# Performance work log

Hardware: AMD Instinct MI355X
Metric: run time of the kernel (lower is better)

The kernel has to match this reference:

```python
import jax, jax.numpy as jnp
import numpy as np

B, L, D, H, DH, M = 2, 2048, 512, 8, 2048, 128  # batch, seq, d_model, heads, d_hidden, max_rel_pos
HD = D // H
EPS = 1e-5


def _ln(x, w, b):
    mu = jnp.mean(x, axis=-1, keepdims=True)
    var = jnp.mean((x - mu) ** 2, axis=-1, keepdims=True)
    return (x - mu) * jax.lax.rsqrt(var + EPS) * w + b


def setup_inputs() -> dict:
    key = jax.random.key(0)
    ks = jax.random.split(key, 8)
    s = 0.02  # init std for weights
    return {
        "x": jax.random.normal(ks[0], (B, L, D), jnp.float32),
        "ln1_w": jnp.ones((D,), jnp.float32),
        "ln1_b": jnp.zeros((D,), jnp.float32),
        "qkv_w": jax.random.normal(ks[1], (D, 3 * D), jnp.float32) * s,
        "qkv_b": jnp.zeros((3 * D,), jnp.float32),
        "out_w": jax.random.normal(ks[2], (D, D), jnp.float32) * s,
        "out_b": jnp.zeros((D,), jnp.float32),
        "rel_bias": jax.random.normal(ks[3], (H, 2 * M - 1), jnp.float32) * s,
        "gamma1": 1e-4 * jnp.ones((D,), jnp.float32),
        "ln2_w": jnp.ones((D,), jnp.float32),
        "ln2_b": jnp.zeros((D,), jnp.float32),
        "ffn_in_w": jax.random.normal(ks[4], (D, 2 * DH), jnp.float32) * s,
        "ffn_in_b": jnp.zeros((2 * DH,), jnp.float32),
        "ffn_out_w": jax.random.normal(ks[5], (DH, D), jnp.float32) * s,
        "ffn_out_b": jnp.zeros((D,), jnp.float32),
        "gamma2": 1e-4 * jnp.ones((D,), jnp.float32),
    }


def _forward(x, ln1_w, ln1_b, qkv_w, qkv_b, out_w, out_b, rel_bias, gamma1,
             ln2_w, ln2_b, ffn_in_w, ffn_in_b, ffn_out_w, ffn_out_b, gamma2):
    b, l, d = x.shape
    # --- PreNorm attention with T5-style relative position bias ---
    h = _ln(x, ln1_w, ln1_b)
    qkv = h @ qkv_w + qkv_b                           # [B, L, 3D]
    q, k, v = jnp.split(qkv, 3, axis=-1)
    q = q.reshape(b, l, H, HD)
    k = k.reshape(b, l, H, HD)
    v = v.reshape(b, l, H, HD)
    scale = 1.0 / jnp.sqrt(jnp.asarray(HD, x.dtype))
    scores = jnp.einsum("bqhd,bkhd->bhqk", q, k) * scale   # [B, H, L, L]
    # relative position bias: clip(i - j) indexed into learned table
    ctx = jnp.arange(l)[:, None] - jnp.arange(l)[None, :]
    ctx = jnp.clip(ctx, -(M - 1), M - 1) + (M - 1)          # [L, L] in [0, 2M-2]
    rel = rel_bias[:, ctx]                                  # [H, L, L]
    scores = scores + rel[None]
    attn = jax.nn.softmax(scores, axis=-1)
    o = jnp.einsum("bhqk,bkhd->bqhd", attn, v).reshape(b, l, d)
    o = o @ out_w + out_b
    x = x + o * gamma1                                      # LayerScale residual
    # --- PreNorm GEGLU FFN ---
    h2 = _ln(x, ln2_w, ln2_b)
    ab = h2 @ ffn_in_w + ffn_in_b                           # [B, L, 2*DH]
    a, bgate = jnp.split(ab, 2, axis=-1)
    f = jax.nn.gelu(bgate, approximate=False) * a
    f = f @ ffn_out_w + ffn_out_b
    x = x + f * gamma2
    return x, attn


def reference(x, ln1_w, ln1_b, qkv_w, qkv_b, out_w, out_b, rel_bias, gamma1,
              ln2_w, ln2_b, ffn_in_w, ffn_in_b, ffn_out_w, ffn_out_b, gamma2):
    return _forward(x, ln1_w, ln1_b, qkv_w, qkv_b, out_w, out_b, rel_bias, gamma1,
                    ln2_w, ln2_b, ffn_in_w, ffn_in_b, ffn_out_w, ffn_out_b, gamma2)
```

## Files before the change

### kernel.cpp

```cpp
#include <hip/hip_runtime.h>
#include <math.h>

typedef __attribute__((ext_vector_type(4))) float f32x4;
typedef __attribute__((ext_vector_type(8))) short bf16x8;
typedef __attribute__((ext_vector_type(4))) short s16x4;

#if __has_builtin(__builtin_amdgcn_exp2f)
#define EXP2(x) __builtin_amdgcn_exp2f(x)
#else
#define EXP2(x) exp2f(x)
#endif

__device__ __forceinline__ unsigned short f2bf(float f) {
  union { float f; unsigned u; } v; v.f = f;
  return (unsigned short)((v.u + 0x7fffu + ((v.u >> 16) & 1u)) >> 16);
}

__global__ void ln_kernel(const float* __restrict__ in, const float* __restrict__ w,
                          const float* __restrict__ b, unsigned short* __restrict__ out) {
  __shared__ float sh[4];
  const int t = threadIdx.x;
  const float* p = in + (size_t)blockIdx.x * 512;
  float a0 = p[t], a1 = p[t + 256];
  float s = a0 + a1;
#pragma unroll
  for (int o = 32; o; o >>= 1) s += __shfl_down(s, o);
  if ((t & 63) == 0) sh[t >> 6] = s;
  __syncthreads();
  s = sh[0] + sh[1] + sh[2] + sh[3];
  float mu = s * (1.0f / 512.0f);
  float d0 = a0 - mu, d1 = a1 - mu;
  float q = d0 * d0 + d1 * d1;
  __syncthreads();
#pragma unroll
  for (int o = 32; o; o >>= 1) q += __shfl_down(q, o);
  if ((t & 63) == 0) sh[t >> 6] = q;
  __syncthreads();
  q = sh[0] + sh[1] + sh[2] + sh[3];
  float rstd = rsqrtf(q * (1.0f / 512.0f) + 1e-5f);
  unsigned short* po = out + (size_t)blockIdx.x * 512;
  po[t]       = f2bf(d0 * rstd * w[t] + b[t]);
  po[t + 256] = f2bf(d1 * rstd * w[t + 256] + b[t + 256]);
}

__global__ void transpose_all(const float* __restrict__ w0, unsigned short* __restrict__ o0,
                              const float* __restrict__ w1, unsigned short* __restrict__ o1,
                              const float* __restrict__ w2, unsigned short* __restrict__ o2,
                              const float* __restrict__ w3, unsigned short* __restrict__ o3) {
  __shared__ float tile[32][33];
  int idx = blockIdx.x;
  const float* in; unsigned short* out; int ldi, ldo, nx;
  if (idx < 768)        { in = w0; out = o0; ldi = 1536; ldo = 512;  nx = 48; }
  else if (idx < 1024)  { idx -= 768;  in = w1; out = o1; ldi = 512;  ldo = 512;  nx = 16; }
  else if (idx < 3072)  { idx -= 1024; in = w2; out = o2; ldi = 4096; ldo = 512;  nx = 128; }
  else                  { idx -= 3072; in = w3; out = o3; ldi = 512;  ldo = 2048; nx = 16; }
  const int tx = threadIdx.x & 31;
  const int ty = threadIdx.x >> 5;
  const int n0 = (idx % nx) * 32, k0 = (idx / nx) * 32;
#pragma unroll
  for (int i = 0; i < 4; ++i)
    tile[ty + i * 8][tx] = in[(size_t)(k0 + ty + i * 8) * ldi + n0 + tx];
  __syncthreads();
#pragma unroll
  for (int i = 0; i < 4; ++i)
    out[(size_t)(n0 + ty + i * 8) * ldo + k0 + tx] = f2bf(tile[tx][ty + i * 8]);
}

template <int WM, int WN, int TM, int TN, int EPI>
__global__ __launch_bounds__(256) void gemm_bb(
    const unsigned short* __restrict__ A, const unsigned short* __restrict__ Bt,
    float* __restrict__ C, unsigned short* __restrict__ Cbf, unsigned short* __restrict__ Vt,
    int K, int lda, int ldb, int ldc,
    const float* __restrict__ bias, const float* __restrict__ resid,
    const float* __restrict__ gamma) {
  constexpr int BM = WM * TM * 16;
  constexpr int BN = WN * TN * 16;
  constexpr int LDS_STRIDE = 72;
  __shared__ short As[BM * LDS_STRIDE];
  __shared__ short Bs[BN * LDS_STRIDE];

  const int tid = threadIdx.x;
  const int m0 = blockIdx.y * BM, n0 = blockIdx.x * BN;
  const int w = tid >> 6, lane = tid & 63;
  const int wm = w / WN, wn = w % WN;
  const int lrow = lane & 15, lq = lane >> 4;

  f32x4 acc[TM][TN];
#pragma unroll
  for (int i = 0; i < TM; ++i)
#pragma unroll
    for (int j = 0; j < TN; ++j) acc[i][j] = (f32x4){0.f, 0.f, 0.f, 0.f};

  for (int k0 = 0; k0 < K; k0 += 64) {
    __syncthreads();
#pragma unroll
    for (int it = 0; it < BM / 32; ++it) {
      int c = it * 256 + tid;
      int row = c >> 3, col = (c & 7) << 3;
      *(bf16x8*)(As + row * LDS_STRIDE + col) =
          *(const bf16x8*)(A + (size_t)(m0 + row) * lda + k0 + col);
    }
#pragma unroll
    for (int it = 0; it < BN / 32; ++it) {
      int c = it * 256 + tid;
      int row = c >> 3, col = (c & 7) << 3;
      *(bf16x8*)(Bs + row * LDS_STRIDE + col) =
          *(const bf16x8*)(Bt + (size_t)(n0 + row) * ldb + k0 + col);
    }
    __syncthreads();

    bf16x8 af[TM][2], bf[TN][2];
#pragma unroll
    for (int mi = 0; mi < TM; ++mi)
#pragma unroll
      for (int c = 0; c < 2; ++c)
        af[mi][c] = *(const bf16x8*)(As + (wm * TM * 16 + mi * 16 + lrow) * LDS_STRIDE + c * 32 + lq * 8);
#pragma unroll
    for (int nj = 0; nj < TN; ++nj)
#pragma unroll
      for (int c = 0; c < 2; ++c)
        bf[nj][c] = *(const bf16x8*)(Bs + (wn * TN * 16 + nj * 16 + lrow) * LDS_STRIDE + c * 32 + lq * 8);
#pragma unroll
    for (int mi = 0; mi < TM; ++mi)
#pragma unroll
      for (int nj = 0; nj < TN; ++nj)
#pragma unroll
        for (int c = 0; c < 2; ++c)
          acc[mi][nj] = __builtin_amdgcn_mfma_f32_16x16x32_bf16(af[mi][c], bf[nj][c], acc[mi][nj], 0, 0, 0);
  }

#pragma unroll
  for (int mi = 0; mi < TM; ++mi) {
#pragma unroll
    for (int nj = 0; nj < TN; ++nj) {
      int gm0 = m0 + wm * TM * 16 + mi * 16 + lq * 4;
      int gn = n0 + wn * TN * 16 + nj * 16 + lrow;
      if constexpr (EPI == 4) {
        if (gn >= 1024) {
          int h = (gn - 1024) >> 6, dd = (gn - 1024) & 63;
          int bb = gm0 >> 11, l0 = gm0 & 2047;
          float bs = bias[gn];
          s16x4 r4 = {(short)f2bf(acc[mi][nj][0] + bs), (short)f2bf(acc[mi][nj][1] + bs),
                      (short)f2bf(acc[mi][nj][2] + bs), (short)f2bf(acc[mi][nj][3] + bs)};
          *(s16x4*)(Vt + ((size_t)(bb * 8 + h) * 64 + dd) * 2048 + l0) = r4;
          continue;
        }
      }
#pragma unroll
      for (int r = 0; r < 4; ++r) {
        int gm = gm0 + r;
        size_t idx = (size_t)gm * ldc + gn;
        float v = acc[mi][nj][r];
        if constexpr (EPI == 0) {
          C[idx] = v + bias[gn];
        } else if constexpr (EPI == 4) {
          float u = v + bias[gn];
          Cbf[idx] = f2bf(gn < 512 ? u * 0.18033688011112042f : u);
        } else {
          C[idx] = resid[idx] + (v + bias[gn]) * gamma[gn];
        }
      }
    }
  }
}

__global__ __launch_bounds__(256) void ffn1_gate_kernel(
    const unsigned short* __restrict__ A, const unsigned short* __restrict__ Bt,
    unsigned short* __restrict__ F, const float* __restrict__ bias) {
  constexpr int LDS_STRIDE = 72;
  __shared__ short As[128 * LDS_STRIDE];
  __shared__ short Bs[64 * LDS_STRIDE];
  __shared__ short Bs2[64 * LDS_STRIDE];

  const int tid = threadIdx.x;
  const int n0 = blockIdx.x * 64, m0 = blockIdx.y * 128;
  const int w = tid >> 6, lane = tid & 63;
  const int wm = w >> 1, wn = w & 1;
  const int lrow = lane & 15, lq = lane >> 4;

  f32x4 acca[4][2], accb[4][2];
#pragma unroll
  for (int i = 0; i < 4; ++i)
#pragma unroll
    for (int j = 0; j < 2; ++j) {
      acca[i][j] = (f32x4){0.f, 0.f, 0.f, 0.f};
      accb[i][j] = (f32x4){0.f, 0.f, 0.f, 0.f};
    }

  for (int k0 = 0; k0 < 512; k0 += 64) {
    __syncthreads();
#pragma unroll
    for (int it = 0; it < 4; ++it) {
      int c = it * 256 + tid;
      int row = c >> 3, col = (c & 7) << 3;
      *(bf16x8*)(As + row * LDS_STRIDE + col) =
          *(const bf16x8*)(A + (size_t)(m0 + row) * 512 + k0 + col);
    }
#pragma unroll
    for (int it = 0; it < 2; ++it) {
      int c = it * 256 + tid;
      int row = c >> 3, col = (c & 7) << 3;
      *(bf16x8*)(Bs + row * LDS_STRIDE + col) =
          *(const bf16x8*)(Bt + (size_t)(n0 + row) * 512 + k0 + col);
      *(bf16x8*)(Bs2 + row * LDS_STRIDE + col) =
          *(const bf16x8*)(Bt + (size_t)(2048 + n0 + row) * 512 + k0 + col);
    }
    __syncthreads();

    bf16x8 af[4][2], ba[2][2], bb[2][2];
#pragma unroll
    for (int mi = 0; mi < 4; ++mi)
#pragma unroll
      for (int c = 0; c < 2; ++c)
        af[mi][c] = *(const bf16x8*)(As + (wm * 64 + mi * 16 + lrow) * LDS_STRIDE + c * 32 + lq * 8);
#pragma unroll
    for (int nj = 0; nj < 2; ++nj)
#pragma unroll
      for (int c = 0; c < 2; ++c) {
        ba[nj][c] = *(const bf16x8*)(Bs + (wn * 32 + nj * 16 + lrow) * LDS_STRIDE + c * 32 + lq * 8);
        bb[nj][c] = *(const bf16x8*)(Bs2 + (wn * 32 + nj * 16 + lrow) * LDS_STRIDE + c * 32 + lq * 8);
      }
#pragma unroll
    for (int mi = 0; mi < 4; ++mi)
#pragma unroll
      for (int nj = 0; nj < 2; ++nj)
#pragma unroll
        for (int c = 0; c < 2; ++c) {
          acca[mi][nj] = __builtin_amdgcn_mfma_f32_16x16x32_bf16(af[mi][c], ba[nj][c], acca[mi][nj], 0, 0, 0);
          accb[mi][nj] = __builtin_amdgcn_mfma_f32_16x16x32_bf16(af[mi][c], bb[nj][c], accb[mi][nj], 0, 0, 0);
        }
  }

#pragma unroll
  for (int mi = 0; mi < 4; ++mi)
#pragma unroll
    for (int nj = 0; nj < 2; ++nj) {
      int gm0 = m0 + wm * 64 + mi * 16 + lq * 4;
      int gn = n0 + wn * 32 + nj * 16 + lrow;
#pragma unroll
      for (int r = 0; r < 4; ++r) {
        float a = acca[mi][nj][r] + bias[gn];
        float bg = accb[mi][nj][r] + bias[2048 + gn];
        float g = 0.5f * bg * (1.0f + erff(bg * 0.70710678118654752f));
        F[(size_t)(gm0 + r) * 2048 + gn] = f2bf(g * a);
      }
    }
}

__global__ __launch_bounds__(256, 8) void attn_fused(
    const unsigned short* __restrict__ qkvbf, const unsigned short* __restrict__ vt,
    const float* __restrict__ rel, float* __restrict__ attn, unsigned short* __restrict__ o) {
  __shared__ __align__(16) float scr[3072];
  __shared__ float erel[256];
  __shared__ float rsum[16];
  __shared__ float rinv[16];

  const int tid = threadIdx.x;
  const int flat = blockIdx.y * 128 + blockIdx.x;
  const int swz = (flat & 7) * 256 + (flat >> 3);
  const int bh = swz >> 7;
  const int m0 = (swz & 127) * 16;
  const int b = bh >> 3, h = bh & 7;

  const int w = tid >> 6, lane = tid & 63;
  const int lrow = lane & 15, lq = lane >> 4;

  const unsigned short* qb = qkvbf + (size_t)(b * 2048) * 1536 + h * 64;
  const unsigned short* kb = qb + 512;
  const unsigned short* vb = vt + (size_t)bh * 64 * 2048;
  float* ab = attn + (size_t)bh * 2048 * 2048;
  const float* relh = rel + h * 255;

  if (tid < 16) rsum[tid] = 0.f;
  if (tid < 255) erel[tid] = __expf(relh[tid]);

  bf16x8 qf[2];
#pragma unroll
  for (int c = 0; c < 2; ++c)
    qf[c] = *(const bf16x8*)(qb + (size_t)(m0 + lrow) * 1536 + c * 32 + lq * 8);

  const unsigned short* krow = kb + (size_t)(w * 32 + lrow) * 1536 + lq * 8;
  const unsigned short* vrow = vb + (size_t)lrow * 2048 + w * 32 + lq * 8;

  __syncthreads();

  float psum[4] = {0.f, 0.f, 0.f, 0.f};
  const int dbase = (m0 + lq * 4) - (w * 32 + lrow);
  for (int t = 0; t < 16; ++t) {
    const int kt0 = t * 128;
    f32x4 acc[2];
#pragma unroll
    for (int nj = 0; nj < 2; ++nj) acc[nj] = (f32x4){0.f, 0.f, 0.f, 0.f};
#pragma unroll
    for (int c = 0; c < 2; ++c) {
      bf16x8 kf[2];
#pragma unroll
      for (int nj = 0; nj < 2; ++nj)
        kf[nj] = *(const bf16x8*)(krow + (size_t)(kt0 + nj * 16) * 1536 + c * 32);
#pragma unroll
      for (int nj = 0; nj < 2; ++nj)
        acc[nj] = __builtin_amdgcn_mfma_f32_16x16x32_bf16(qf[c], kf[nj], acc[nj], 0, 0, 0);
    }
    const int Dt = m0 - kt0;
    if (Dt >= 254 || Dt <= -144) {
      float ec = erel[Dt >= 254 ? 254 : 0];
#pragma unroll
      for (int r = 0; r < 4; ++r)
        psum[r] += ec * (EXP2(acc[0][r]) + EXP2(acc[1][r]));
    } else {
#pragma unroll
      for (int nj = 0; nj < 2; ++nj) {
        int d0 = dbase - kt0 - nj * 16;
#pragma unroll
        for (int r = 0; r < 4; ++r) {
          int d = d0 + r;
          d = d < -127 ? -127 : (d > 127 ? 127 : d);
          psum[r] += EXP2(acc[nj][r]) * erel[d + 127];
        }
      }
    }
  }
#pragma unroll
  for (int off = 1; off < 16; off <<= 1)
#pragma unroll
    for (int r = 0; r < 4; ++r) psum[r] += __shfl_xor(psum[r], off);
  if (lrow == 0) {
#pragma unroll
    for (int r = 0; r < 4; ++r) atomicAdd(&rsum[lq * 4 + r], psum[r]);
  }
  __syncthreads();
  if (tid < 16) rinv[tid] = 1.0f / rsum[tid];
  __syncthreads();
  float rv[4];
#pragma unroll
  for (int r = 0; r < 4; ++r) rv[r] = rinv[lq * 4 + r];

  f32x4 oacc[4];
#pragma unroll
  for (int nj = 0; nj < 4; ++nj) oacc[nj] = (f32x4){0.f, 0.f, 0.f, 0.f};
  float* pw = scr + w * 512;
  const int wsw = lq << 3;
  const int rsw = ((lrow >> 2) & 3) << 3;

  for (int t = 0; t < 16; ++t) {
    const int kt0 = t * 128;
    f32x4 acc[2];
#pragma unroll
    for (int nj = 0; nj < 2; ++nj) acc[nj] = (f32x4){0.f, 0.f, 0.f, 0.f};
#pragma unroll
    for (int c = 0; c < 2; ++c) {
      bf16x8 kf[2];
#pragma unroll
      for (int nj = 0; nj < 2; ++nj)
        kf[nj] = *(const bf16x8*)(krow + (size_t)(kt0 + nj * 16) * 1536 + c * 32);
#pragma unroll
      for (int nj = 0; nj < 2; ++nj)
        acc[nj] = __builtin_amdgcn_mfma_f32_16x16x32_bf16(qf[c], kf[nj], acc[nj], 0, 0, 0);
    }

    const int Dt = m0 - kt0;
    if (Dt >= 254 || Dt <= -144) {
      float ec = erel[Dt >= 254 ? 254 : 0];
#pragma unroll
      for (int r = 0; r < 4; ++r) {
        float fr = ec * rv[r];
        int prow = lq * 4 + r;
#pragma unroll
        for (int nj = 0; nj < 2; ++nj)
          pw[prow * 32 + ((nj * 16 + lrow) ^ wsw)] = EXP2(acc[nj][r]) * fr;
      }
    } else {
#pragma unroll
      for (int r = 0; r < 4; ++r) {
        int prow = lq * 4 + r;
        int d0 = dbase - kt0 + r;
#pragma unroll
        for (int nj = 0; nj < 2; ++nj) {
          int d = d0 - nj * 16;
          d = d < -127 ? -127 : (d > 127 ? 127 : d);
          pw[prow * 32 + ((nj * 16 + lrow) ^ wsw)] = EXP2(acc[nj][r]) * (erel[d + 127] * rv[r]);
        }
      }
    }

#pragma unroll
    for (int it = 0; it < 2; ++it) {
      int unit = it * 64 + lane;
      int row = unit >> 3, cg = unit & 7;
      f32x4 vv = *(const f32x4*)(pw + row * 32 + ((cg * 4) ^ (((row >> 2) & 3) << 3)));
      __builtin_nontemporal_store(
          vv, (f32x4*)(ab + (size_t)(m0 + row) * 2048 + kt0 + w * 32 + cg * 4));
    }

    {
      const float* pp = pw + lrow * 32 + ((lq * 8) ^ rsw);
      f32x4 pa = *(const f32x4*)pp;
      f32x4 pb = *(const f32x4*)(pp + 4);
      bf16x8 ap = {(short)f2bf(pa[0]), (short)f2bf(pa[1]), (short)f2bf(pa[2]), (short)f2bf(pa[3]),
                   (short)f2bf(pb[0]), (short)f2bf(pb[1]), (short)f2bf(pb[2]), (short)f2bf(pb[3])};
      bf16x8 bv[4];
#pragma unroll
      for (int nj = 0; nj < 4; ++nj)
        bv[nj] = *(const bf16x8*)(vrow + (size_t)(nj * 16) * 2048 + kt0);
#pragma unroll
      for (int nj = 0; nj < 4; ++nj)
        oacc[nj] = __builtin_amdgcn_mfma_f32_16x16x32_bf16(ap, bv[nj], oacc[nj], 0, 0, 0);
    }
  }

  __syncthreads();
  if (w > 0) {
#pragma unroll
    for (int nj = 0; nj < 4; ++nj)
#pragma unroll
      for (int r = 0; r < 4; ++r)
        scr[(w - 1) * 1024 + (lq * 4 + r) * 64 + nj * 16 + lrow] = oacc[nj][r];
  }
  __syncthreads();
  if (w == 0) {
#pragma unroll
    for (int nj = 0; nj < 4; ++nj)
#pragma unroll
      for (int r = 0; r < 4; ++r) {
        int ii = (lq * 4 + r) * 64 + nj * 16 + lrow;
        float v = oacc[nj][r] + scr[ii] + scr[1024 + ii] + scr[2048 + ii];
        o[(size_t)(b * 2048 + m0 + lq * 4 + r) * 512 + h * 64 + nj * 16 + lrow] = f2bf(v);
      }
  }
}

extern "C" void kernel_launch(void* const* d_in, const int* in_sizes, int n_in,
                              void* d_out, int out_size, void* d_ws, size_t ws_size,
                              hipStream_t stream) {
  (void)in_sizes; (void)n_in; (void)out_size; (void)ws_size;
  const float* x        = (const float*)d_in[0];
  const float* ln1_w    = (const float*)d_in[1];
  const float* ln1_b    = (const float*)d_in[2];
  const float* qkv_w    = (const float*)d_in[3];
  const float* qkv_b    = (const float*)d_in[4];
  const float* out_w    = (const float*)d_in[5];
  const float* out_b    = (const float*)d_in[6];
  const float* rel_bias = (const float*)d_in[7];
  const float* gamma1   = (const float*)d_in[8];
  const float* ln2_w    = (const float*)d_in[9];
  const float* ln2_b    = (const float*)d_in[10];
  const float* ffn_in_w = (const float*)d_in[11];
  const float* ffn_in_b = (const float*)d_in[12];
  const float* ffn_out_w  = (const float*)d_in[13];
  const float* ffn_out_b  = (const float*)d_in[14];
  const float* gamma2   = (const float*)d_in[15];

  float* x_out = (float*)d_out;
  float* attn  = x_out + (size_t)2 * 2048 * 512;

  float* ws  = (float*)d_ws;
  float* x1  = ws;
  unsigned short* h_bf  = (unsigned short*)(x1 + 2097152);
  unsigned short* o_bf  = h_bf + 2097152;
  unsigned short* f_bf  = o_bf + 2097152;
  unsigned short* qkvbf = f_bf;
  unsigned short* bt_qkv  = f_bf + 8388608;
  unsigned short* bt_out  = bt_qkv + 786432;
  unsigned short* bt_ffn1 = bt_out + 262144;
  unsigned short* bt_ffn2 = bt_ffn1 + 2097152;
  unsigned short* vt      = bt_ffn2 + 1048576;

  transpose_all<<<4096, 256, 0, stream>>>(qkv_w, bt_qkv, out_w, bt_out,
                                          ffn_in_w, bt_ffn1, ffn_out_w, bt_ffn2);

  ln_kernel<<<4096, 256, 0, stream>>>(x, ln1_w, ln1_b, h_bf);

  gemm_bb<2, 2, 4, 2, 4><<<dim3(24, 32, 1), 256, 0, stream>>>(
      h_bf, bt_qkv, nullptr, qkvbf, vt, 512, 512, 512, 1536, qkv_b, nullptr, nullptr);

  attn_fused<<<dim3(128, 16, 1), 256, 0, stream>>>(qkvbf, vt, rel_bias, attn, o_bf);

  gemm_bb<2, 2, 2, 2, 3><<<dim3(8, 64, 1), 256, 0, stream>>>(
      o_bf, bt_out, x1, nullptr, nullptr, 512, 512, 512, 512, out_b, x, gamma1);

  ln_kernel<<<4096, 256, 0, stream>>>(x1, ln2_w, ln2_b, h_bf);

  ffn1_gate_kernel<<<dim3(32, 32, 1), 256, 0, stream>>>(h_bf, bt_ffn1, f_bf, ffn_in_b);

  gemm_bb<2, 2, 2, 2, 3><<<dim3(8, 64, 1), 256, 0, stream>>>(
      f_bf, bt_ffn2, x_out, nullptr, nullptr, 2048, 2048, 2048, 512, ffn_out_b, x1, gamma2);
}
```

Before: 583.7 us.

## Enlarge attention tile to 32 query rows with 2x2 warp layout and K prefetch

The fused attention kernel now processes 32 query rows per block instead of 16. Its four waves are arranged 2x2: two row groups, each splitting the 128-key tile into two 64-key halves. K fragments are double-buffered in registers so the next tile's loads are issued before the current tile's MFMAs, and the final reduction across waves merges only two partials. This halves redundant K/V reads per query row and hides load latency. In exchange it uses more registers, which is why launch bounds drop to 4 blocks per CU, and the grid halves.

After: 591.9 us. About the same (+1.4%).

```diff
diff --git a/kernel.cpp b/kernel.cpp
--- a/kernel.cpp
+++ b/kernel.cpp
@@ -247,22 +247,23 @@
     }
 }
 
-__global__ __launch_bounds__(256, 8) void attn_fused(
+__global__ __launch_bounds__(256, 4) void attn_fused(
     const unsigned short* __restrict__ qkvbf, const unsigned short* __restrict__ vt,
     const float* __restrict__ rel, float* __restrict__ attn, unsigned short* __restrict__ o) {
-  __shared__ __align__(16) float scr[3072];
+  __shared__ __align__(16) float p_f32[4 * 16 * 64];
   __shared__ float erel[256];
-  __shared__ float rsum[16];
-  __shared__ float rinv[16];
+  __shared__ float rsum[32];
+  __shared__ float rinv[32];
 
   const int tid = threadIdx.x;
-  const int flat = blockIdx.y * 128 + blockIdx.x;
-  const int swz = (flat & 7) * 256 + (flat >> 3);
-  const int bh = swz >> 7;
-  const int m0 = (swz & 127) * 16;
+  const int flat = blockIdx.y * 64 + blockIdx.x;
+  const int swz = (flat & 7) * 128 + (flat >> 3);
+  const int bh = swz >> 6;
+  const int m0 = (swz & 63) * 32;
   const int b = bh >> 3, h = bh & 7;
 
   const int w = tid >> 6, lane = tid & 63;
+  const int wm = w >> 1, wn = w & 1;
   const int lrow = lane & 15, lq = lane >> 4;
 
   const unsigned short* qb = qkvbf + (size_t)(b * 2048) * 1536 + h * 64;
@@ -271,45 +272,53 @@
   float* ab = attn + (size_t)bh * 2048 * 2048;
   const float* relh = rel + h * 255;
 
-  if (tid < 16) rsum[tid] = 0.f;
+  if (tid < 32) rsum[tid] = 0.f;
   if (tid < 255) erel[tid] = __expf(relh[tid]);
 
   bf16x8 qf[2];
 #pragma unroll
   for (int c = 0; c < 2; ++c)
-    qf[c] = *(const bf16x8*)(qb + (size_t)(m0 + lrow) * 1536 + c * 32 + lq * 8);
-
-  const unsigned short* krow = kb + (size_t)(w * 32 + lrow) * 1536 + lq * 8;
-  const unsigned short* vrow = vb + (size_t)lrow * 2048 + w * 32 + lq * 8;
-
-  __syncthreads();
+    qf[c] = *(const bf16x8*)(qb + (size_t)(m0 + wm * 16 + lrow) * 1536 + c * 32 + lq * 8);
+
+  const unsigned short* krow = kb + (size_t)(wn * 64 + lrow) * 1536 + lq * 8;
+  const unsigned short* vrow = vb + (size_t)lrow * 2048 + wn * 64 + lq * 8;
+
+  __syncthreads();
+
+  auto LDK = [&](int t, bf16x8 (&kf)[2][4]) {
+#pragma unroll
+    for (int c = 0; c < 2; ++c)
+#pragma unroll
+      for (int nj = 0; nj < 4; ++nj)
+        kf[c][nj] = *(const bf16x8*)(krow + (size_t)(t * 128 + nj * 16) * 1536 + c * 32);
+  };
 
   float psum[4] = {0.f, 0.f, 0.f, 0.f};
-  const int dbase = (m0 + lq * 4) - (w * 32 + lrow);
-  for (int t = 0; t < 16; ++t) {
+  const int dbase = (m0 + wm * 16 + lq * 4) - (wn * 64 + lrow);
+
+  auto P1 = [&](int t, bf16x8 (&kf)[2][4]) {
     const int kt0 = t * 128;
-    f32x4 acc[2];
-#pragma unroll
-    for (int nj = 0; nj < 2; ++nj) acc[nj] = (f32x4){0.f, 0.f, 0.f, 0.f};
-#pragma unroll
-    for (int c = 0; c < 2; ++c) {
-      bf16x8 kf[2];
-#pragma unroll
-      for (int nj = 0; nj < 2; ++nj)
-        kf[nj] = *(const bf16x8*)(krow + (size_t)(kt0 + nj * 16) * 1536 + c * 32);
-#pragma unroll
-      for (int nj = 0; nj < 2; ++nj)
-        acc[nj] = __builtin_amdgcn_mfma_f32_16x16x32_bf16(qf[c], kf[nj], acc[nj], 0, 0, 0);
-    }
+    f32x4 acc[4];
+#pragma unroll
+    for (int nj = 0; nj < 4; ++nj) acc[nj] = (f32x4){0.f, 0.f, 0.f, 0.f};
+#pragma unroll
+    for (int c = 0; c < 2; ++c)
+#pragma unroll
+      for (int nj = 0; nj < 4; ++nj)
+        acc[nj] = __builtin_amdgcn_mfma_f32_16x16x32_bf16(qf[c], kf[c][nj], acc[nj], 0, 0, 0);
     const int Dt = m0 - kt0;
-    if (Dt >= 254 || Dt <= -144) {
-      float ec = erel[Dt >= 254 ? 254 : 0];
-#pragma unroll
-      for (int r = 0; r < 4; ++r)
-        psum[r] += ec * (EXP2(acc[0][r]) + EXP2(acc[1][r]));
+    if (Dt >= 256 || Dt <= -160) {
+      float ec = erel[Dt >= 256 ? 254 : 0];
+#pragma unroll
+      for (int r = 0; r < 4; ++r) {
+        float s = 0.f;
+#pragma unroll
+        for (int nj = 0; nj < 4; ++nj) s += EXP2(acc[nj][r]);
+        psum[r] += ec * s;
+      }
     } else {
 #pragma unroll
-      for (int nj = 0; nj < 2; ++nj) {
+      for (int nj = 0; nj < 4; ++nj) {
         int d0 = dbase - kt0 - nj * 16;
 #pragma unroll
         for (int r = 0; r < 4; ++r) {
@@ -319,55 +328,63 @@
         }
       }
     }
-  }
+  };
+
+  {
+    bf16x8 kA[2][4], kB[2][4];
+    LDK(0, kA);
+#pragma unroll 1
+    for (int tt = 0; tt < 8; ++tt) {
+      LDK(2 * tt + 1, kB);
+      P1(2 * tt, kA);
+      if (tt < 7) LDK(2 * tt + 2, kA);
+      P1(2 * tt + 1, kB);
+    }
+  }
+
 #pragma unroll
   for (int off = 1; off < 16; off <<= 1)
 #pragma unroll
     for (int r = 0; r < 4; ++r) psum[r] += __shfl_xor(psum[r], off);
   if (lrow == 0) {
 #pragma unroll
-    for (int r = 0; r < 4; ++r) atomicAdd(&rsum[lq * 4 + r], psum[r]);
-  }
-  __syncthreads();
-  if (tid < 16) rinv[tid] = 1.0f / rsum[tid];
+    for (int r = 0; r < 4; ++r) atomicAdd(&rsum[wm * 16 + lq * 4 + r], psum[r]);
+  }
+  __syncthreads();
+  if (tid < 32) rinv[tid] = 1.0f / rsum[tid];
   __syncthreads();
   float rv[4];
 #pragma unroll
-  for (int r = 0; r < 4; ++r) rv[r] = rinv[lq * 4 + r];
+  for (int r = 0; r < 4; ++r) rv[r] = rinv[wm * 16 + lq * 4 + r];
 
   f32x4 oacc[4];
 #pragma unroll
   for (int nj = 0; nj < 4; ++nj) oacc[nj] = (f32x4){0.f, 0.f, 0.f, 0.f};
-  float* pw = scr + w * 512;
-  const int wsw = lq << 3;
-  const int rsw = ((lrow >> 2) & 3) << 3;
-
-  for (int t = 0; t < 16; ++t) {
+  float* pw = p_f32 + w * (16 * 64);
+  const int wsw = lq << 4;
+  const int rsw = ((lrow >> 2) & 3) << 4;
+
+  auto P2 = [&](int t, bf16x8 (&kf)[2][4]) {
     const int kt0 = t * 128;
-    f32x4 acc[2];
-#pragma unroll
-    for (int nj = 0; nj < 2; ++nj) acc[nj] = (f32x4){0.f, 0.f, 0.f, 0.f};
-#pragma unroll
-    for (int c = 0; c < 2; ++c) {
-      bf16x8 kf[2];
-#pragma unroll
-      for (int nj = 0; nj < 2; ++nj)
-        kf[nj] = *(const bf16x8*)(krow + (size_t)(kt0 + nj * 16) * 1536 + c * 32);
-#pragma unroll
-      for (int nj = 0; nj < 2; ++nj)
-        acc[nj] = __builtin_amdgcn_mfma_f32_16x16x32_bf16(qf[c], kf[nj], acc[nj], 0, 0, 0);
-    }
+    f32x4 acc[4];
+#pragma unroll
+    for (int nj = 0; nj < 4; ++nj) acc[nj] = (f32x4){0.f, 0.f, 0.f, 0.f};
+#pragma unroll
+    for (int c = 0; c < 2; ++c)
+#pragma unroll
+      for (int nj = 0; nj < 4; ++nj)
+        acc[nj] = __builtin_amdgcn_mfma_f32_16x16x32_bf16(qf[c], kf[c][nj], acc[nj], 0, 0, 0);
 
     const int Dt = m0 - kt0;
-    if (Dt >= 254 || Dt <= -144) {
-      float ec = erel[Dt >= 254 ? 254 : 0];
+    if (Dt >= 256 || Dt <= -160) {
+      float ec = erel[Dt >= 256 ? 254 : 0];
 #pragma unroll
       for (int r = 0; r < 4; ++r) {
         float fr = ec * rv[r];
         int prow = lq * 4 + r;
 #pragma unroll
-        for (int nj = 0; nj < 2; ++nj)
-          pw[prow * 32 + ((nj * 16 + lrow) ^ wsw)] = EXP2(acc[nj][r]) * fr;
+        for (int nj = 0; nj < 4; ++nj)
+          pw[prow * 64 + ((nj * 16 + lrow) ^ wsw)] = EXP2(acc[nj][r]) * fr;
       }
     } else {
 #pragma unroll
@@ -375,25 +392,25 @@
         int prow = lq * 4 + r;
         int d0 = dbase - kt0 + r;
 #pragma unroll
-        for (int nj = 0; nj < 2; ++nj) {
+        for (int nj = 0; nj < 4; ++nj) {
           int d = d0 - nj * 16;
           d = d < -127 ? -127 : (d > 127 ? 127 : d);
-          pw[prow * 32 + ((nj * 16 + lrow) ^ wsw)] = EXP2(acc[nj][r]) * (erel[d + 127] * rv[r]);
+          pw[prow * 64 + ((nj * 16 + lrow) ^ wsw)] = EXP2(acc[nj][r]) * (erel[d + 127] * rv[r]);
         }
       }
     }
 
 #pragma unroll
-    for (int it = 0; it < 2; ++it) {
-      int unit = it * 64 + lane;
-      int row = unit >> 3, cg = unit & 7;
-      f32x4 vv = *(const f32x4*)(pw + row * 32 + ((cg * 4) ^ (((row >> 2) & 3) << 3)));
+    for (int it = 0; it < 4; ++it) {
+      int rr = lq * 4 + it;
+      f32x4 vv = *(const f32x4*)(pw + rr * 64 + ((lrow * 4) ^ wsw));
       __builtin_nontemporal_store(
-          vv, (f32x4*)(ab + (size_t)(m0 + row) * 2048 + kt0 + w * 32 + cg * 4));
-    }
-
-    {
-      const float* pp = pw + lrow * 32 + ((lq * 8) ^ rsw);
+          vv, (f32x4*)(ab + (size_t)(m0 + wm * 16 + rr) * 2048 + kt0 + wn * 64 + lrow * 4));
+    }
+
+#pragma unroll
+    for (int c2 = 0; c2 < 2; ++c2) {
+      const float* pp = pw + lrow * 64 + ((c2 * 32 + lq * 8) ^ rsw);
       f32x4 pa = *(const f32x4*)pp;
       f32x4 pb = *(const f32x4*)(pp + 4);
       bf16x8 ap = {(short)f2bf(pa[0]), (short)f2bf(pa[1]), (short)f2bf(pa[2]), (short)f2bf(pa[3]),
@@ -401,30 +418,43 @@
       bf16x8 bv[4];
 #pragma unroll
       for (int nj = 0; nj < 4; ++nj)
-        bv[nj] = *(const bf16x8*)(vrow + (size_t)(nj * 16) * 2048 + kt0);
+        bv[nj] = *(const bf16x8*)(vrow + (size_t)(nj * 16) * 2048 + kt0 + c2 * 32);
 #pragma unroll
       for (int nj = 0; nj < 4; ++nj)
         oacc[nj] = __builtin_amdgcn_mfma_f32_16x16x32_bf16(ap, bv[nj], oacc[nj], 0, 0, 0);
     }
-  }
-
-  __syncthreads();
-  if (w > 0) {
+  };
+
+  {
+    bf16x8 kA[2][4], kB[2][4];
+    LDK(0, kA);
+#pragma unroll 1
+    for (int tt = 0; tt < 8; ++tt) {
+      LDK(2 * tt + 1, kB);
+      P2(2 * tt, kA);
+      if (tt < 7) LDK(2 * tt + 2, kA);
+      P2(2 * tt + 1, kB);
+    }
+  }
+
+  __syncthreads();
+  float* osc = p_f32;
+  if (wn == 0) {
 #pragma unroll
     for (int nj = 0; nj < 4; ++nj)
 #pragma unroll
       for (int r = 0; r < 4; ++r)
-        scr[(w - 1) * 1024 + (lq * 4 + r) * 64 + nj * 16 + lrow] = oacc[nj][r];
-  }
-  __syncthreads();
-  if (w == 0) {
+        osc[(wm * 16 + lq * 4 + r) * 64 + nj * 16 + lrow] = oacc[nj][r];
+  }
+  __syncthreads();
+  if (wn == 1) {
 #pragma unroll
     for (int nj = 0; nj < 4; ++nj)
 #pragma unroll
       for (int r = 0; r < 4; ++r) {
-        int ii = (lq * 4 + r) * 64 + nj * 16 + lrow;
-        float v = oacc[nj][r] + scr[ii] + scr[1024 + ii] + scr[2048 + ii];
-        o[(size_t)(b * 2048 + m0 + lq * 4 + r) * 512 + h * 64 + nj * 16 + lrow] = f2bf(v);
+        int rr = m0 + wm * 16 + lq * 4 + r;
+        float v = oacc[nj][r] + osc[(wm * 16 + lq * 4 + r) * 64 + nj * 16 + lrow];
+        o[(size_t)(b * 2048 + rr) * 512 + h * 64 + nj * 16 + lrow] = f2bf(v);
       }
   }
 }
@@ -473,7 +503,7 @@
   gemm_bb<2, 2, 4, 2, 4><<<dim3(24, 32, 1), 256, 0, stream>>>(
       h_bf, bt_qkv, nullptr, qkvbf, vt, 512, 512, 512, 1536, qkv_b, nullptr, nullptr);
 
-  attn_fused<<<dim3(128, 16, 1), 256, 0, stream>>>(qkvbf, vt, rel_bias, attn, o_bf);
+  attn_fused<<<dim3(64, 16, 1), 256, 0, stream>>>(qkvbf, vt, rel_bias, attn, o_bf);
 
   gemm_bb<2, 2, 2, 2, 3><<<dim3(8, 64, 1), 256, 0, stream>>>(
       o_bf, bt_out, x1, nullptr, nullptr, 512, 512, 512, 512, out_b, x, gamma1);
```
